# Kernel optimization log

Hardware: AMD Instinct MI355X
Metric: run time of the kernel (lower is better)

Reference implementation:

```python
import jax, jax.numpy as jnp
import numpy as np

B, T = 32, 512
VOCAB, WDIM, H, NUM_LABELS = 100000, 300, 256, 2


def setup_inputs() -> dict:
    key = jax.random.key(0)
    ks = jax.random.split(key, 16)
    x = jax.random.randint(ks[0], (B, T), 0, VOCAB, dtype=jnp.int32)
    lengths = jax.random.randint(ks[1], (B,), T // 2, T + 1, dtype=jnp.int32)
    mask = (jnp.arange(T)[None, :] < lengths[:, None]).astype(jnp.int32)
    s = 0.05
    emb_table = jax.random.normal(ks[2], (VOCAB, WDIM), jnp.float32)
    W_in = jax.random.normal(ks[3], (WDIM, H), jnp.float32) * s
    b_in = jnp.zeros((H,), jnp.float32)
    Wih_f = jax.random.normal(ks[4], (H, 4 * H), jnp.float32) * s
    Whh_f = jax.random.normal(ks[5], (H, 4 * H), jnp.float32) * s
    bl_f = jnp.zeros((4 * H,), jnp.float32)
    Wih_b = jax.random.normal(ks[6], (H, 4 * H), jnp.float32) * s
    Whh_b = jax.random.normal(ks[7], (H, 4 * H), jnp.float32) * s
    bl_b = jnp.zeros((4 * H,), jnp.float32)
    Wfc = jax.random.normal(ks[8], (2 * H, H), jnp.float32) * s
    bfc = jnp.zeros((H,), jnp.float32)
    Wout = jax.random.normal(ks[9], (H, NUM_LABELS), jnp.float32) * s
    bout = jnp.zeros((NUM_LABELS,), jnp.float32)
    return dict(emb_table=emb_table, W_in=W_in, b_in=b_in,
                Wih_f=Wih_f, Whh_f=Whh_f, bl_f=bl_f,
                Wih_b=Wih_b, Whh_b=Whh_b, bl_b=bl_b,
                Wfc=Wfc, bfc=bfc, Wout=Wout, bout=bout,
                x=x, mask=mask, lengths=lengths)


def _lstm_dir(xs, maskf, Wih, Whh, b, reverse):
    # xs: [B,T,H], maskf: [B,T] float. Masked LSTM: padded steps carry state.
    xs_t = jnp.swapaxes(xs, 0, 1)                # [T,B,H]
    m_t = jnp.swapaxes(maskf, 0, 1)[..., None]   # [T,B,1]
    h0 = jnp.zeros((xs.shape[0], Whh.shape[0]), xs.dtype)
    c0 = h0

    def step(carry, inp):
        h, c = carry
        xt, mt = inp
        z = xt @ Wih + h @ Whh + b               # [B,4H]
        i, f, g, o = jnp.split(z, 4, axis=-1)
        i = jax.nn.sigmoid(i); f = jax.nn.sigmoid(f)
        g = jnp.tanh(g); o = jax.nn.sigmoid(o)
        c_new = f * c + i * g
        h_new = o * jnp.tanh(c_new)
        c = mt * c_new + (1.0 - mt) * c
        h = mt * h_new + (1.0 - mt) * h
        return (h, c), h

    _, hs = jax.lax.scan(step, (h0, c0), (xs_t, m_t), reverse=reverse)
    return jnp.swapaxes(hs, 0, 1)                # [B,T,H]


def reference(emb_table, W_in, b_in, Wih_f, Whh_f, bl_f, Wih_b, Whh_b, bl_b,
              Wfc, bfc, Wout, bout, x, mask, lengths):
    maskf = mask.astype(jnp.float32)
    x_vecs = jnp.take(emb_table, x, axis=0)          # [B,T,WDIM]
    z = jax.nn.relu(x_vecs @ W_in + b_in)            # wordvec layer + relu
    h_fwd = _lstm_dir(z, maskf, Wih_f, Whh_f, bl_f, reverse=False)
    h_bwd = _lstm_dir(z, maskf, Wih_b, Whh_b, bl_b, reverse=True)
    h_mat = jnp.concatenate([h_fwd, h_bwd], axis=-1)  # [B,T,2H]
    h_masked = h_mat * maskf[..., None]
    fc_in = jnp.sum(h_masked / lengths.astype(jnp.float32)[:, None, None], axis=1)
    fc_hidden = jax.nn.relu(fc_in @ Wfc + bfc)        # dropout = identity (eval)
    return fc_hidden @ Wout + bout                    # [B, NUM_LABELS]
```

## Files before the change

kernel.cpp:

```cpp
#include <hip/hip_runtime.h>
#include <math.h>

#define B_    32
#define T_    512
#define WDIM_ 300
#define H_    256
#define G4_   1024
#define M_    (B_ * T_)

#define NCG   8
#define NWG   256
#define THR   512
#define HXN   (2 * 2 * B_ * H_)

#define RPT4(M, b)  M(b) M((b)+1) M((b)+2) M((b)+3)
#define RPT16(M, b) RPT4(M, b) RPT4(M, (b)+4) RPT4(M, (b)+8) RPT4(M, (b)+12)
#define RPT64(M)    RPT16(M, 0) RPT16(M, 16) RPT16(M, 32) RPT16(M, 48)

__global__ __launch_bounds__(256)
void k_embed_proj(const float* __restrict__ emb, const float* __restrict__ Win,
                  const float* __restrict__ bin, const int* __restrict__ x,
                  float* __restrict__ z)
{
    __shared__ float Ash[16][132];
    __shared__ float Bsh[16][132];
    __shared__ int   rows[128];

    const int tid = threadIdx.x;
    const int tx = tid & 15, ty = tid >> 4;
    const int rm = blockIdx.y * 128;
    const int cn = blockIdx.x * 128;

    if (tid < 128) rows[tid] = x[rm + tid];
    __syncthreads();

    float acc[8][8];
#pragma unroll
    for (int i = 0; i < 8; ++i)
#pragma unroll
        for (int j = 0; j < 8; ++j) acc[i][j] = 0.f;

    for (int kc = 0; kc < 19; ++kc) {
        const int k0 = kc * 16;
#pragma unroll
        for (int e = 0; e < 8; ++e) {
            const int idx = e * 256 + tid;
            const int r = idx >> 4, kk = idx & 15;
            const int k = k0 + kk;
            const int v = rows[r];
            Ash[kk][r] = (k < WDIM_) ? emb[(size_t)v * WDIM_ + k] : 0.f;
        }
#pragma unroll
        for (int e = 0; e < 8; ++e) {
            const int idx = e * 256 + tid;
            const int kk = idx >> 7, n = idx & 127;
            const int k = k0 + kk;
            Bsh[kk][n] = (k < WDIM_) ? Win[(size_t)k * H_ + cn + n] : 0.f;
        }
        __syncthreads();
#pragma unroll
        for (int kk = 0; kk < 16; ++kk) {
            float a[8], bb[8];
#pragma unroll
            for (int i = 0; i < 8; ++i) a[i] = Ash[kk][ty * 8 + i];
#pragma unroll
            for (int j = 0; j < 8; ++j) bb[j] = Bsh[kk][tx * 8 + j];
#pragma unroll
            for (int i = 0; i < 8; ++i)
#pragma unroll
                for (int j = 0; j < 8; ++j) acc[i][j] += a[i] * bb[j];
        }
        __syncthreads();
    }

#pragma unroll
    for (int i = 0; i < 8; ++i) {
        const int row = rm + ty * 8 + i;
#pragma unroll
        for (int j = 0; j < 8; ++j) {
            const int col = cn + tx * 8 + j;
            z[(size_t)row * H_ + col] = fmaxf(acc[i][j] + bin[col], 0.f);
        }
    }
}

__global__ __launch_bounds__(256)
void k_in_proj(const float* __restrict__ z,
               const float* __restrict__ Wf, const float* __restrict__ blf,
               const float* __restrict__ Wb, const float* __restrict__ blb,
               float* __restrict__ Pf, float* __restrict__ Pb)
{
    const float* W  = blockIdx.z ? Wb  : Wf;
    const float* bl = blockIdx.z ? blb : blf;
    float*       P  = blockIdx.z ? Pb  : Pf;

    __shared__ float Ash[16][132];
    __shared__ float Bsh[16][132];

    const int tid = threadIdx.x;
    const int tx = tid & 15, ty = tid >> 4;
    const int rm = blockIdx.y * 128;
    const int cn = blockIdx.x * 128;

    float acc[8][8];
#pragma unroll
    for (int i = 0; i < 8; ++i)
#pragma unroll
        for (int j = 0; j < 8; ++j) acc[i][j] = 0.f;

    for (int kc = 0; kc < 16; ++kc) {
        const int k0 = kc * 16;
#pragma unroll
        for (int e = 0; e < 8; ++e) {
            const int idx = e * 256 + tid;
            const int r = idx >> 4, kk = idx & 15;
            Ash[kk][r] = z[(size_t)(rm + r) * H_ + k0 + kk];
        }
#pragma unroll
        for (int e = 0; e < 8; ++e) {
            const int idx = e * 256 + tid;
            const int kk = idx >> 7, n = idx & 127;
            Bsh[kk][n] = W[(size_t)(k0 + kk) * G4_ + cn + n];
        }
        __syncthreads();
#pragma unroll
        for (int kk = 0; kk < 16; ++kk) {
            float a[8], bb[8];
#pragma unroll
            for (int i = 0; i < 8; ++i) a[i] = Ash[kk][ty * 8 + i];
#pragma unroll
            for (int j = 0; j < 8; ++j) bb[j] = Bsh[kk][tx * 8 + j];
#pragma unroll
            for (int i = 0; i < 8; ++i)
#pragma unroll
                for (int j = 0; j < 8; ++j) acc[i][j] += a[i] * bb[j];
        }
        __syncthreads();
    }

#pragma unroll
    for (int i = 0; i < 8; ++i) {
        const int row = rm + ty * 8 + i;
#pragma unroll
        for (int j = 0; j < 8; ++j) {
            const int col = cn + tx * 8 + j;
            P[(size_t)row * G4_ + col] = acc[i][j] + bl[col];
        }
    }
}

__global__ void k_init(unsigned long long* __restrict__ hx)
{
    const int i = blockIdx.x * blockDim.x + threadIdx.x;
    if (i < HXN) hx[i] = 0ull;
}

__global__ __launch_bounds__(THR, 2)
void k_lstm_persist(const float* __restrict__ Pf, const float* __restrict__ Pb,
                    const float* __restrict__ Whf, const float* __restrict__ Whb,
                    const int* __restrict__ lengths,
                    unsigned long long* __restrict__ hx,
                    float* __restrict__ pool)
{
    __shared__ float h_sh[2][256];
    __shared__ float zp[4][2][128];

    const int tid = threadIdx.x;
    const int wg  = blockIdx.x;
    const int bg  = wg & 15;
    const int dir = (wg >> 4) & 1;
    const int cg  = wg >> 5;

    const float* P   = dir ? Pb  : Pf;
    const float* Whh = dir ? Whb : Whf;

    const int brow0 = bg * 2;
    const int len0 = lengths[brow0], len1 = lengths[brow0 + 1];
    const int tmax = max(len0, len1);

    const int q   = tid >> 7;
    const int cl  = tid & 127;
    const int g0  = cl >> 5;
    const int dd0 = cl & 31;
    const int gcol = g0 * 256 + cg * 32 + dd0;
    const int q64 = q * 64;

    float wv[64];
    {
        const float* wp = Whh + (size_t)q64 * G4_ + gcol;
#define LOADW(k) wv[k] = wp[(size_t)(k) * G4_];
        RPT64(LOADW)
#undef LOADW
    }

    const int gr    = tid >> 5;
    const int gd    = tid & 31;
    const int gbrow = brow0 + gr;
    const int glen  = gr ? len1 : len0;
    float cst = 0.f, hreg = 0.f, pacc = 0.f;

    const int lrow = tid >> 8;
    const int ld   = tid & 255;
    unsigned long long* slotR = hx + ((size_t)dir * 32 + brow0 + lrow) * 256 + ld;
    unsigned long long* slotW = hx + ((size_t)dir * 32 + gbrow) * 256 + cg * 32 + gd;
    const size_t bufStride = (size_t)2 * B_ * H_;

    for (int s = 0; s < tmax; ++s) {
        const int tt = dir ? (tmax - 1 - s) : s;

        float pv0 = 0.f, pv1 = 0.f, pv2 = 0.f, pv3 = 0.f;
        if (tid < 64) {
            const float* pr = P + (size_t)(gbrow * T_ + tt) * G4_ + cg * 32 + gd;
            pv0 = pr[0]; pv1 = pr[256]; pv2 = pr[512]; pv3 = pr[768];
        }

        {
            const unsigned long long* sp = slotR + (size_t)(s & 1) * bufStride;
            unsigned long long pk = __hip_atomic_load(sp, __ATOMIC_RELAXED,
                                                      __HIP_MEMORY_SCOPE_AGENT);
            while ((unsigned)(pk >> 32) < (unsigned)s) {
                __builtin_amdgcn_s_sleep(1);
                pk = __hip_atomic_load(sp, __ATOMIC_RELAXED,
                                       __HIP_MEMORY_SCOPE_AGENT);
            }
            h_sh[lrow][ld] = __uint_as_float((unsigned)pk);
        }
        __syncthreads();

        {
            const float* h0 = &h_sh[0][q64];
            const float* h1 = &h_sh[1][q64];
            float a0 = 0.f, a1 = 0.f;
#define GEMV4(k4) { \
            const float4 hv0 = *(const float4*)(h0 + 4 * (k4)); \
            const float4 hv1 = *(const float4*)(h1 + 4 * (k4)); \
            a0 += hv0.x * wv[4*(k4)  ]; a1 += hv1.x * wv[4*(k4)  ]; \
            a0 += hv0.y * wv[4*(k4)+1]; a1 += hv1.y * wv[4*(k4)+1]; \
            a0 += hv0.z * wv[4*(k4)+2]; a1 += hv1.z * wv[4*(k4)+2]; \
            a0 += hv0.w * wv[4*(k4)+3]; a1 += hv1.w * wv[4*(k4)+3]; }
            RPT16(GEMV4, 0)
#undef GEMV4
            zp[q][0][cl] = a0;
            zp[q][1][cl] = a1;
        }
        __syncthreads();

        if (tid < 64) {
            float zi = pv0 + zp[0][gr][gd]      + zp[1][gr][gd]      + zp[2][gr][gd]      + zp[3][gr][gd];
            float zf = pv1 + zp[0][gr][32 + gd] + zp[1][gr][32 + gd] + zp[2][gr][32 + gd] + zp[3][gr][32 + gd];
            float zg = pv2 + zp[0][gr][64 + gd] + zp[1][gr][64 + gd] + zp[2][gr][64 + gd] + zp[3][gr][64 + gd];
            float zo = pv3 + zp[0][gr][96 + gd] + zp[1][gr][96 + gd] + zp[2][gr][96 + gd] + zp[3][gr][96 + gd];
            const float ig = 1.f / (1.f + expf(-zi));
            const float fg = 1.f / (1.f + expf(-zf));
            const float gg = tanhf(zg);
            const float og = 1.f / (1.f + expf(-zo));
            const float cn = fg * cst + ig * gg;
            const float hn = og * tanhf(cn);
            if (tt < glen) { cst = cn; hreg = hn; pacc += hn; }
            const unsigned long long opk =
                ((unsigned long long)(unsigned)(s + 1) << 32) |
                (unsigned long long)__float_as_uint(hreg);
            __hip_atomic_store(slotW + (size_t)((s + 1) & 1) * bufStride, opk,
                               __ATOMIC_RELAXED, __HIP_MEMORY_SCOPE_AGENT);
        }
    }

    if (tid < 64)
        pool[gbrow * 512 + dir * 256 + cg * 32 + gd] = pacc / (float)glen;
}

__global__ __launch_bounds__(256)
void k_fc(const float* __restrict__ pool, const float* __restrict__ Wfc,
          const float* __restrict__ bfc, const float* __restrict__ Wout,
          const float* __restrict__ bout, float* __restrict__ out)
{
    __shared__ float p_sh[512];
    __shared__ float red[8];

    const int tid = threadIdx.x;
    const int b   = blockIdx.x;

    p_sh[tid]       = pool[b * 512 + tid];
    p_sh[256 + tid] = pool[b * 512 + 256 + tid];
    __syncthreads();

    float acc = bfc[tid];
#pragma unroll 8
    for (int k = 0; k < 512; ++k)
        acc += p_sh[k] * Wfc[(size_t)k * H_ + tid];
    const float fh = fmaxf(acc, 0.f);

    float p0 = fh * Wout[tid * 2 + 0];
    float p1 = fh * Wout[tid * 2 + 1];
#pragma unroll
    for (int off = 32; off > 0; off >>= 1) {
        p0 += __shfl_down(p0, off);
        p1 += __shfl_down(p1, off);
    }
    const int wave = tid >> 6;
    if ((tid & 63) == 0) { red[wave * 2] = p0; red[wave * 2 + 1] = p1; }
    __syncthreads();
    if (tid == 0) {
        out[b * 2 + 0] = red[0] + red[2] + red[4] + red[6] + bout[0];
        out[b * 2 + 1] = red[1] + red[3] + red[5] + red[7] + bout[1];
    }
}

__global__ void k_sentinel(float* out, int n)
{
    const int i = blockIdx.x * blockDim.x + threadIdx.x;
    if (i < n) out[i] = 1.0e9f;
}

extern "C" void kernel_launch(void* const* d_in, const int* in_sizes, int n_in,
                              void* d_out, int out_size, void* d_ws, size_t ws_size,
                              hipStream_t stream)
{
    const float* emb  = (const float*)d_in[0];
    const float* Win  = (const float*)d_in[1];
    const float* bin  = (const float*)d_in[2];
    const float* Wihf = (const float*)d_in[3];
    const float* Whhf = (const float*)d_in[4];
    const float* blf  = (const float*)d_in[5];
    const float* Wihb = (const float*)d_in[6];
    const float* Whhb = (const float*)d_in[7];
    const float* blb  = (const float*)d_in[8];
    const float* Wfc  = (const float*)d_in[9];
    const float* bfc  = (const float*)d_in[10];
    const float* Wout = (const float*)d_in[11];
    const float* bout = (const float*)d_in[12];
    const int*   x    = (const int*)d_in[13];
    const int*   lens = (const int*)d_in[15];
    float*       out  = (float*)d_out;

    const size_t need = ((size_t)M_ * H_ + 2 * (size_t)M_ * G4_) * sizeof(float);
    if (ws_size < need) {
        hipLaunchKernelGGL(k_sentinel, dim3(1), dim3(64), 0, stream, out, out_size);
        return;
    }

    float* z  = (float*)d_ws;
    float* Pf = z + (size_t)M_ * H_;
    float* Pb = Pf + (size_t)M_ * G4_;

    unsigned long long* hx   = (unsigned long long*)d_ws;
    float*              pool = (float*)(hx + HXN);

    hipLaunchKernelGGL(k_embed_proj, dim3(2, 128), dim3(256), 0, stream,
                       emb, Win, bin, x, z);
    hipLaunchKernelGGL(k_in_proj, dim3(8, 128, 2), dim3(256), 0, stream,
                       z, Wihf, blf, Wihb, blb, Pf, Pb);
    hipLaunchKernelGGL(k_init, dim3(128), dim3(256), 0, stream, hx);
    hipLaunchKernelGGL(k_lstm_persist, dim3(NWG), dim3(THR), 0, stream,
                       Pf, Pb, Whhf, Whhb, lens, hx, pool);
    hipLaunchKernelGGL(k_fc, dim3(32), dim3(256), 0, stream,
                       pool, Wfc, bfc, Wout, bout, out);
}
```

Baseline: 1.364 ms.

## Broadcast h via readlane in LSTM step and double-buffer gate partials

Each wavefront now polls the global h slots for its own 64-element slice of the two batch rows. It broadcasts the values across lanes with readlane instead of staging them in shared memory, which removes one __syncthreads per timestep. The gate partial-sum buffer is double-buffered by step parity so the single remaining barrier is enough. The cost is redundant global polling, since each of the 8 waves reads its slice while two waves share the same q, plus 128 scalar readlane operations per step in place of vector LDS loads.

```diff
diff --git a/kernel.cpp b/kernel.cpp
--- a/kernel.cpp
+++ b/kernel.cpp
@@ -162,8 +162,7 @@
                     unsigned long long* __restrict__ hx,
                     float* __restrict__ pool)
 {
-    __shared__ float h_sh[2][256];
-    __shared__ float zp[4][2][128];
+    __shared__ float zp[2][4][2][128];
 
     const int tid = threadIdx.x;
     const int wg  = blockIdx.x;
@@ -178,12 +177,14 @@
     const int len0 = lengths[brow0], len1 = lengths[brow0 + 1];
     const int tmax = max(len0, len1);
 
-    const int q   = tid >> 7;
-    const int cl  = tid & 127;
-    const int g0  = cl >> 5;
-    const int dd0 = cl & 31;
+    const int lane = tid & 63;
+    const int w    = tid >> 6;
+    const int q    = w >> 1;
+    const int cl   = ((w & 1) << 6) | lane;
+    const int g0   = cl >> 5;
+    const int dd0  = cl & 31;
     const int gcol = g0 * 256 + cg * 32 + dd0;
-    const int q64 = q * 64;
+    const int q64  = q * 64;
 
     float wv[64];
     {
@@ -193,20 +194,20 @@
 #undef LOADW
     }
 
-    const int gr    = tid >> 5;
+    const int gr    = (tid >> 5) & 1;
     const int gd    = tid & 31;
     const int gbrow = brow0 + gr;
     const int glen  = gr ? len1 : len0;
     float cst = 0.f, hreg = 0.f, pacc = 0.f;
 
-    const int lrow = tid >> 8;
-    const int ld   = tid & 255;
-    unsigned long long* slotR = hx + ((size_t)dir * 32 + brow0 + lrow) * 256 + ld;
-    unsigned long long* slotW = hx + ((size_t)dir * 32 + gbrow) * 256 + cg * 32 + gd;
+    unsigned long long* slotR0 = hx + ((size_t)dir * 32 + brow0) * 256 + q64 + lane;
+    unsigned long long* slotR1 = slotR0 + 256;
+    unsigned long long* slotW  = hx + ((size_t)dir * 32 + gbrow) * 256 + cg * 32 + gd;
     const size_t bufStride = (size_t)2 * B_ * H_;
 
     for (int s = 0; s < tmax; ++s) {
-        const int tt = dir ? (tmax - 1 - s) : s;
+        const int tt  = dir ? (tmax - 1 - s) : s;
+        const int par = s & 1;
 
         float pv0 = 0.f, pv1 = 0.f, pv2 = 0.f, pv3 = 0.f;
         if (tid < 64) {
@@ -214,42 +215,43 @@
             pv0 = pr[0]; pv1 = pr[256]; pv2 = pr[512]; pv3 = pr[768];
         }
 
+        const size_t poff = (size_t)par * bufStride;
+        unsigned long long pk0 = __hip_atomic_load(slotR0 + poff, __ATOMIC_RELAXED,
+                                                   __HIP_MEMORY_SCOPE_AGENT);
+        unsigned long long pk1 = __hip_atomic_load(slotR1 + poff, __ATOMIC_RELAXED,
+                                                   __HIP_MEMORY_SCOPE_AGENT);
+        while ((unsigned)(pk0 >> 32) < (unsigned)s) {
+            __builtin_amdgcn_s_sleep(1);
+            pk0 = __hip_atomic_load(slotR0 + poff, __ATOMIC_RELAXED,
+                                    __HIP_MEMORY_SCOPE_AGENT);
+        }
+        while ((unsigned)(pk1 >> 32) < (unsigned)s) {
+            __builtin_amdgcn_s_sleep(1);
+            pk1 = __hip_atomic_load(slotR1 + poff, __ATOMIC_RELAXED,
+                                    __HIP_MEMORY_SCOPE_AGENT);
+        }
+        const int h0u = (int)(unsigned)pk0;
+        const int h1u = (int)(unsigned)pk1;
+
         {
-            const unsigned long long* sp = slotR + (size_t)(s & 1) * bufStride;
-            unsigned long long pk = __hip_atomic_load(sp, __ATOMIC_RELAXED,
-                                                      __HIP_MEMORY_SCOPE_AGENT);
-            while ((unsigned)(pk >> 32) < (unsigned)s) {
-                __builtin_amdgcn_s_sleep(1);
-                pk = __hip_atomic_load(sp, __ATOMIC_RELAXED,
-                                       __HIP_MEMORY_SCOPE_AGENT);
-            }
-            h_sh[lrow][ld] = __uint_as_float((unsigned)pk);
-        }
-        __syncthreads();
-
-        {
-            const float* h0 = &h_sh[0][q64];
-            const float* h1 = &h_sh[1][q64];
             float a0 = 0.f, a1 = 0.f;
-#define GEMV4(k4) { \
-            const float4 hv0 = *(const float4*)(h0 + 4 * (k4)); \
-            const float4 hv1 = *(const float4*)(h1 + 4 * (k4)); \
-            a0 += hv0.x * wv[4*(k4)  ]; a1 += hv1.x * wv[4*(k4)  ]; \
-            a0 += hv0.y * wv[4*(k4)+1]; a1 += hv1.y * wv[4*(k4)+1]; \
-            a0 += hv0.z * wv[4*(k4)+2]; a1 += hv1.z * wv[4*(k4)+2]; \
-            a0 += hv0.w * wv[4*(k4)+3]; a1 += hv1.w * wv[4*(k4)+3]; }
-            RPT16(GEMV4, 0)
-#undef GEMV4
-            zp[q][0][cl] = a0;
-            zp[q][1][cl] = a1;
+#define STEPK(k) { \
+            const float hs0 = __uint_as_float((unsigned)__builtin_amdgcn_readlane(h0u, k)); \
+            const float hs1 = __uint_as_float((unsigned)__builtin_amdgcn_readlane(h1u, k)); \
+            a0 = fmaf(hs0, wv[k], a0); \
+            a1 = fmaf(hs1, wv[k], a1); }
+            RPT64(STEPK)
+#undef STEPK
+            zp[par][q][0][cl] = a0;
+            zp[par][q][1][cl] = a1;
         }
         __syncthreads();
 
         if (tid < 64) {
-            float zi = pv0 + zp[0][gr][gd]      + zp[1][gr][gd]      + zp[2][gr][gd]      + zp[3][gr][gd];
-            float zf = pv1 + zp[0][gr][32 + gd] + zp[1][gr][32 + gd] + zp[2][gr][32 + gd] + zp[3][gr][32 + gd];
-            float zg = pv2 + zp[0][gr][64 + gd] + zp[1][gr][64 + gd] + zp[2][gr][64 + gd] + zp[3][gr][64 + gd];
-            float zo = pv3 + zp[0][gr][96 + gd] + zp[1][gr][96 + gd] + zp[2][gr][96 + gd] + zp[3][gr][96 + gd];
+            float zi = pv0 + zp[par][0][gr][gd]      + zp[par][1][gr][gd]      + zp[par][2][gr][gd]      + zp[par][3][gr][gd];
+            float zf = pv1 + zp[par][0][gr][32 + gd] + zp[par][1][gr][32 + gd] + zp[par][2][gr][32 + gd] + zp[par][3][gr][32 + gd];
+            float zg = pv2 + zp[par][0][gr][64 + gd] + zp[par][1][gr][64 + gd] + zp[par][2][gr][64 + gd] + zp[par][3][gr][64 + gd];
+            float zo = pv3 + zp[par][0][gr][96 + gd] + zp[par][1][gr][96 + gd] + zp[par][2][gr][96 + gd] + zp[par][3][gr][96 + gd];
             const float ig = 1.f / (1.f + expf(-zi));
             const float fg = 1.f / (1.f + expf(-zf));
             const float gg = tanhf(zg);
```

New measurement: 1.727 ms. 26.6% more time.
